# Performance work log

Measured on AMD Instinct MI355X. Metric: run time of the kernel, lower is better.

Reference implementation:

```python
import jax, jax.numpy as jnp
import numpy as np

GRID = 192
ISO = 0.0

CORNERS = [(0,0,0),(1,0,0),(0,1,0),(1,1,0),(0,0,1),(1,0,1),(0,1,1),(1,1,1)]
# 12 cube edges as pairs of corner offsets
EDGES = [
    ((0,0,0),(1,0,0)),((0,1,0),(1,1,0)),((0,0,1),(1,0,1)),((0,1,1),(1,1,1)),
    ((0,0,0),(0,1,0)),((1,0,0),(1,1,0)),((0,0,1),(0,1,1)),((1,0,1),(1,1,1)),
    ((0,0,0),(0,0,1)),((1,0,0),(1,0,1)),((0,1,0),(0,1,1)),((1,1,0),(1,1,1)),
]


def setup_inputs() -> dict:
    key = jax.random.key(0)
    grid = jax.random.normal(key, (GRID, GRID, GRID), dtype=jnp.float32)
    return {"grid": grid}


def _dual_verts(grid, iso):
    # One dual vertex per cell of the padded grid: mean of the iso-crossing
    # points on the cell's 12 edges (dual-marching-cubes vertex placement).
    X, Y, Z = grid.shape
    P = jnp.pad(grid, 1, constant_values=iso + 1.0)  # (X+2, Y+2, Z+2)
    Cx, Cy, Cz = X + 1, Y + 1, Z + 1                 # number of cells per axis
    vals = {c: P[c[0]:c[0]+Cx, c[1]:c[1]+Cy, c[2]:c[2]+Cz] for c in CORNERS}
    sum_pt = jnp.zeros((Cx, Cy, Cz, 3), grid.dtype)
    cnt = jnp.zeros((Cx, Cy, Cz), grid.dtype)
    for ca, cb in EDGES:  # fixed 12-iteration loop, fully vectorized over cells
        vA, vB = vals[ca], vals[cb]
        m = (vA < iso) != (vB < iso)                 # edge crosses isosurface
        t = jnp.where(m, (iso - vA) / jnp.where(m, vB - vA, 1.0), 0.0)
        oa = jnp.asarray(ca, grid.dtype)
        ob = jnp.asarray(cb, grid.dtype)
        pt = oa + t[..., None] * (ob - oa)           # local crossing point
        mf = m.astype(grid.dtype)
        sum_pt = sum_pt + mf[..., None] * pt
        cnt = cnt + mf
    base = jnp.stack(jnp.meshgrid(jnp.arange(Cx), jnp.arange(Cy), jnp.arange(Cz), indexing='ij'), axis=-1).astype(grid.dtype)
    verts = base + sum_pt / jnp.maximum(cnt, 1.0)[..., None]
    # undo +1 padding offset, then normalize by (dim - 1) as in the module
    verts = (verts - 1.0) / (jnp.asarray([X, Y, Z], grid.dtype) - 1.0)
    return verts.reshape(-1, 3), (cnt > 0).reshape(-1)


def _quads(grid, iso):
    # One quad per grid edge that crosses the isosurface, connecting the dual
    # vertices of the 4 cells sharing that edge. Emitted densely with a mask
    # (jit-compatible fixed shapes); masked rows are inactive.
    X, Y, Z = grid.shape
    P = jnp.pad(grid, 1, constant_values=iso + 1.0)
    Cx, Cy, Cz = X + 1, Y + 1, Z + 1
    sgn = P < iso
    def cid(a, b, c):  # flatten cell index
        return (a * Cy + b) * Cz + c
    qs, ms = [], []
    # x-directed edges: shared by cells (i, j-1/j, k-1/k)
    m = sgn[0:Cx, 1:Cy, 1:Cz] != sgn[1:Cx+1, 1:Cy, 1:Cz]
    a = jnp.arange(Cx)[:, None, None]; b = jnp.arange(1, Cy)[None, :, None]; c = jnp.arange(1, Cz)[None, None, :]
    q = jnp.stack(jnp.broadcast_arrays(cid(a, b-1, c-1), cid(a, b, c-1), cid(a, b, c), cid(a, b-1, c)), axis=-1)
    qs.append(q.reshape(-1, 4)); ms.append(m.reshape(-1))
    # y-directed edges: shared by cells (i-1/i, j, k-1/k)
    m = sgn[1:Cx, 0:Cy, 1:Cz] != sgn[1:Cx, 1:Cy+1, 1:Cz]
    a = jnp.arange(1, Cx)[:, None, None]; b = jnp.arange(Cy)[None, :, None]; c = jnp.arange(1, Cz)[None, None, :]
    q = jnp.stack(jnp.broadcast_arrays(cid(a-1, b, c-1), cid(a, b, c-1), cid(a, b, c), cid(a-1, b, c)), axis=-1)
    qs.append(q.reshape(-1, 4)); ms.append(m.reshape(-1))
    # z-directed edges: shared by cells (i-1/i, j-1/j, k)
    m = sgn[1:Cx, 1:Cy, 0:Cz] != sgn[1:Cx, 1:Cy, 1:Cz+1]
    a = jnp.arange(1, Cx)[:, None, None]; b = jnp.arange(1, Cy)[None, :, None]; c = jnp.arange(Cz)[None, None, :]
    q = jnp.stack(jnp.broadcast_arrays(cid(a-1, b-1, c), cid(a, b-1, c), cid(a, b, c), cid(a-1, b, c)), axis=-1)
    qs.append(q.reshape(-1, 4)); ms.append(m.reshape(-1))
    quads = jnp.concatenate(qs, axis=0).astype(jnp.int32)
    qmask = jnp.concatenate(ms, axis=0)
    return quads, qmask


def reference(grid):
    verts, vmask = _dual_verts(grid, ISO)
    quads, qmask = _quads(grid, ISO)
    return verts, vmask, quads, qmask
```

## Files before the change

kernel.cpp:

```cpp
#include <hip/hip_runtime.h>

#define GN 192
#define CN 193
#define CN2 (CN * CN)

#define NV        ((size_t)CN * CN * CN)
#define OFF_VMASK ((size_t)(NV * 3))
#define OFF_QUADS ((size_t)(OFF_VMASK + NV))
#define QSEG      ((size_t)CN * GN * GN)
#define OFF_QMASK ((size_t)(OFF_QUADS + 3 * QSEG * 4))

__device__ __forceinline__ float gpad(const float* __restrict__ g, int x, int y, int z) {
    if ((unsigned)x < (unsigned)GN && (unsigned)y < (unsigned)GN && (unsigned)z < (unsigned)GN)
        return g[((size_t)x * GN + y) * GN + z];
    return 1.0f;
}

__global__ __launch_bounds__(256) void dmc_fused(const float* __restrict__ g,
                                                 float* __restrict__ out) {
    const size_t lin = (size_t)blockIdx.x * 256 + threadIdx.x;
    if (lin >= NV) return;
    const int linI = (int)lin;
    const int k = linI % CN;
    const int t2 = linI / CN;
    const int j = t2 % CN;
    const int i = t2 / CN;

    const float v000 = gpad(g, i - 1, j - 1, k - 1);
    const float v100 = gpad(g, i,     j - 1, k - 1);
    const float v010 = gpad(g, i - 1, j,     k - 1);
    const float v110 = gpad(g, i,     j,     k - 1);
    const float v001 = gpad(g, i - 1, j - 1, k);
    const float v101 = gpad(g, i,     j - 1, k);
    const float v011 = gpad(g, i - 1, j,     k);
    const float v111 = gpad(g, i,     j,     k);

    const bool s000 = v000 < 0.f, s100 = v100 < 0.f, s010 = v010 < 0.f, s110 = v110 < 0.f;
    const bool s001 = v001 < 0.f, s101 = v101 < 0.f, s011 = v011 < 0.f, s111 = v111 < 0.f;

    float sx = 0.f, sy = 0.f, sz = 0.f;
    int cnt = 0;
    auto acc = [&](float vA, float vB, bool sA, bool sB, int axis, float o1, float o2) {
        if (sA != sB) {
            const float t = -vA * __builtin_amdgcn_rcpf(vB - vA);
            if (axis == 0)      { sx += t;  sy += o1; sz += o2; }
            else if (axis == 1) { sx += o1; sy += t;  sz += o2; }
            else                { sx += o1; sy += o2; sz += t;  }
            cnt++;
        }
    };
    acc(v000, v100, s000, s100, 0, 0.f, 0.f);
    acc(v010, v110, s010, s110, 0, 1.f, 0.f);
    acc(v001, v101, s001, s101, 0, 0.f, 1.f);
    acc(v011, v111, s011, s111, 0, 1.f, 1.f);
    acc(v000, v010, s000, s010, 1, 0.f, 0.f);
    acc(v100, v110, s100, s110, 1, 1.f, 0.f);
    acc(v001, v011, s001, s011, 1, 0.f, 1.f);
    acc(v101, v111, s101, s111, 1, 1.f, 1.f);
    acc(v000, v001, s000, s001, 2, 0.f, 0.f);
    acc(v100, v101, s100, s101, 2, 1.f, 0.f);
    acc(v010, v011, s010, s011, 2, 0.f, 1.f);
    acc(v110, v111, s110, s111, 2, 1.f, 1.f);

    const float rc = __builtin_amdgcn_rcpf(fmaxf((float)cnt, 1.0f));
    const float inv191 = 1.0f / 191.0f;
    out[lin * 3 + 0] = ((float)i + sx * rc - 1.0f) * inv191;
    out[lin * 3 + 1] = ((float)j + sy * rc - 1.0f) * inv191;
    out[lin * 3 + 2] = ((float)k + sz * rc - 1.0f) * inv191;
    out[OFF_VMASK + lin] = (cnt > 0) ? 1.0f : 0.0f;

    const float flin = (float)linI;
    float4* const quads = (float4*)(out + OFF_QUADS);
    float* const qmask = out + OFF_QMASK;

    if (j < GN && k < GN) {
        const size_t r = ((size_t)i * GN + j) * GN + k;
        float4 q;
        q.x = flin;
        q.y = flin + (float)CN;
        q.z = flin + (float)(CN+1);
        q.w = flin + 1.0f;
        quads[r] = q;
        qmask[r] = (s011 != s111) ? 1.0f : 0.0f;
    }
    if (i >= 1 && k < GN) {
        const size_t r = QSEG + ((size_t)(i - 1) * CN + j) * GN + k;
        float4 q;
        q.x = flin - (float)CN2;
        q.y = flin;
        q.z = flin + 1.0f;
        q.w = flin - (float)(CN2 - 1);
        quads[r] = q;
        qmask[r] = (s001 != s011) ? 1.0f : 0.0f;
    }
    if (i >= 1 && j >= 1) {
        const size_t r = 2 * QSEG + ((size_t)(i - 1) * GN + (j - 1)) * CN + k;
        float4 q;
        q.x = flin - (float)(CN2 + CN);
        q.y = flin - (float)CN;
        q.z = flin;
        q.w = flin - (float)CN2;
        quads[r] = q;
        qmask[r] = (s000 != s001) ? 1.0f : 0.0f;
    }
}

extern "C" void kernel_launch(void* const* d_in, const int* in_sizes, int n_in,
                              void* d_out, int out_size, void* d_ws, size_t ws_size,
                              hipStream_t stream) {
    const float* g = (const float*)d_in[0];
    float* out = (float*)d_out;
    const int nblocks = (int)((NV + 255) / 256);
    dmc_fused<<<dim3(nblocks), dim3(256), 0, stream>>>(g, out);
}
```

Baseline: 557.3 us.

## Process four z-adjacent cells per thread with vector loads and nontemporal stores

Each thread now handles a run of four cells along z. It loads four 5-element grid rows with vector loads instead of 8 scalar loads per cell, and shares corner values between neighbouring cells. Quad and mask outputs are written with vector nontemporal stores, aiming to cut load instructions and cache pollution in a store-bound kernel. The cost is wider per-lane store strides, which may reduce per-instruction coalescing, plus more register use.

```diff
diff --git a/kernel.cpp b/kernel.cpp
--- a/kernel.cpp
+++ b/kernel.cpp
@@ -3,6 +3,8 @@
 #define GN 192
 #define CN 193
 #define CN2 (CN * CN)
+#define QPOS 49
+#define NPOS ((size_t)CN * CN * QPOS)
 
 #define NV        ((size_t)CN * CN * CN)
 #define OFF_VMASK ((size_t)(NV * 3))
@@ -10,98 +12,132 @@
 #define QSEG      ((size_t)CN * GN * GN)
 #define OFF_QMASK ((size_t)(OFF_QUADS + 3 * QSEG * 4))
 
-__device__ __forceinline__ float gpad(const float* __restrict__ g, int x, int y, int z) {
-    if ((unsigned)x < (unsigned)GN && (unsigned)y < (unsigned)GN && (unsigned)z < (unsigned)GN)
-        return g[((size_t)x * GN + y) * GN + z];
-    return 1.0f;
+typedef float v4f __attribute__((ext_vector_type(4)));
+
+__device__ __forceinline__ void load_row(const float* __restrict__ g, int x, int y,
+                                         int k0, float r[5]) {
+    if ((unsigned)x < (unsigned)GN && (unsigned)y < (unsigned)GN) {
+        const float* rp = g + ((size_t)x * GN + y) * GN;
+        r[0] = (k0 > 0) ? rp[k0 - 1] : 1.0f;
+        if (k0 < GN) {
+            const v4f v = *(const v4f*)(rp + k0);
+            r[1] = v.x; r[2] = v.y; r[3] = v.z; r[4] = v.w;
+        } else {
+            r[1] = r[2] = r[3] = r[4] = 1.0f;
+        }
+    } else {
+        r[0] = r[1] = r[2] = r[3] = r[4] = 1.0f;
+    }
 }
 
 __global__ __launch_bounds__(256) void dmc_fused(const float* __restrict__ g,
                                                  float* __restrict__ out) {
-    const size_t lin = (size_t)blockIdx.x * 256 + threadIdx.x;
-    if (lin >= NV) return;
-    const int linI = (int)lin;
-    const int k = linI % CN;
-    const int t2 = linI / CN;
-    const int j = t2 % CN;
-    const int i = t2 / CN;
+    const size_t t = (size_t)blockIdx.x * 256 + threadIdx.x;
+    if (t >= NPOS) return;
+    const int ti = (int)t;
+    const int q  = ti % QPOS;
+    const int rj = ti / QPOS;
+    const int j  = rj % CN;
+    const int i  = rj / CN;
+    const int k0 = q * 4;
 
-    const float v000 = gpad(g, i - 1, j - 1, k - 1);
-    const float v100 = gpad(g, i,     j - 1, k - 1);
-    const float v010 = gpad(g, i - 1, j,     k - 1);
-    const float v110 = gpad(g, i,     j,     k - 1);
-    const float v001 = gpad(g, i - 1, j - 1, k);
-    const float v101 = gpad(g, i,     j - 1, k);
-    const float v011 = gpad(g, i - 1, j,     k);
-    const float v111 = gpad(g, i,     j,     k);
+    float r00[5], r10[5], r01[5], r11[5];
+    load_row(g, i - 1, j - 1, k0, r00);
+    load_row(g, i,     j - 1, k0, r10);
+    load_row(g, i - 1, j,     k0, r01);
+    load_row(g, i,     j,     k0, r11);
 
-    const bool s000 = v000 < 0.f, s100 = v100 < 0.f, s010 = v010 < 0.f, s110 = v110 < 0.f;
-    const bool s001 = v001 < 0.f, s101 = v101 < 0.f, s011 = v011 < 0.f, s111 = v111 < 0.f;
+    const int ncell = (q < 48) ? 4 : 1;
+    const int cellbase = rj * CN + k0;
+    const float flin0 = (float)cellbase;
 
-    float sx = 0.f, sy = 0.f, sz = 0.f;
-    int cnt = 0;
-    auto acc = [&](float vA, float vB, bool sA, bool sB, int axis, float o1, float o2) {
-        if (sA != sB) {
-            const float t = -vA * __builtin_amdgcn_rcpf(vB - vA);
-            if (axis == 0)      { sx += t;  sy += o1; sz += o2; }
-            else if (axis == 1) { sx += o1; sy += t;  sz += o2; }
-            else                { sx += o1; sy += o2; sz += t;  }
-            cnt++;
+    float mA[4], mB[4], mC[4];
+
+    #pragma unroll
+    for (int c = 0; c < 4; ++c) {
+        const float v000 = r00[c], v001 = r00[c + 1];
+        const float v100 = r10[c], v101 = r10[c + 1];
+        const float v010 = r01[c], v011 = r01[c + 1];
+        const float v110 = r11[c], v111 = r11[c + 1];
+        const bool s000 = v000 < 0.f, s100 = v100 < 0.f, s010 = v010 < 0.f, s110 = v110 < 0.f;
+        const bool s001 = v001 < 0.f, s101 = v101 < 0.f, s011 = v011 < 0.f, s111 = v111 < 0.f;
+
+        mA[c] = (s011 != s111) ? 1.0f : 0.0f;
+        mB[c] = (s001 != s011) ? 1.0f : 0.0f;
+        mC[c] = (s000 != s001) ? 1.0f : 0.0f;
+
+        float sx = 0.f, sy = 0.f, sz = 0.f;
+        int cnt = 0;
+        auto acc = [&](float vA, float vB, bool sA, bool sB, int axis, float o1, float o2) {
+            if (sA != sB) {
+                const float tt = -vA * __builtin_amdgcn_rcpf(vB - vA);
+                if (axis == 0)      { sx += tt; sy += o1; sz += o2; }
+                else if (axis == 1) { sx += o1; sy += tt; sz += o2; }
+                else                { sx += o1; sy += o2; sz += tt; }
+                cnt++;
+            }
+        };
+        acc(v000, v100, s000, s100, 0, 0.f, 0.f);
+        acc(v010, v110, s010, s110, 0, 1.f, 0.f);
+        acc(v001, v101, s001, s101, 0, 0.f, 1.f);
+        acc(v011, v111, s011, s111, 0, 1.f, 1.f);
+        acc(v000, v010, s000, s010, 1, 0.f, 0.f);
+        acc(v100, v110, s100, s110, 1, 1.f, 0.f);
+        acc(v001, v011, s001, s011, 1, 0.f, 1.f);
+        acc(v101, v111, s101, s111, 1, 1.f, 1.f);
+        acc(v000, v001, s000, s001, 2, 0.f, 0.f);
+        acc(v100, v101, s100, s101, 2, 1.f, 0.f);
+        acc(v010, v011, s010, s011, 2, 0.f, 1.f);
+        acc(v110, v111, s110, s111, 2, 1.f, 1.f);
+
+        if (c < ncell) {
+            const float rc = __builtin_amdgcn_rcpf(fmaxf((float)cnt, 1.0f));
+            const float inv191 = 1.0f / 191.0f;
+            const int k = k0 + c;
+            const size_t vb = (size_t)(cellbase + c) * 3;
+            out[vb + 0] = ((float)i + sx * rc - 1.0f) * inv191;
+            out[vb + 1] = ((float)j + sy * rc - 1.0f) * inv191;
+            out[vb + 2] = ((float)k + sz * rc - 1.0f) * inv191;
+            out[OFF_VMASK + cellbase + c] = (cnt > 0) ? 1.0f : 0.0f;
         }
-    };
-    acc(v000, v100, s000, s100, 0, 0.f, 0.f);
-    acc(v010, v110, s010, s110, 0, 1.f, 0.f);
-    acc(v001, v101, s001, s101, 0, 0.f, 1.f);
-    acc(v011, v111, s011, s111, 0, 1.f, 1.f);
-    acc(v000, v010, s000, s010, 1, 0.f, 0.f);
-    acc(v100, v110, s100, s110, 1, 1.f, 0.f);
-    acc(v001, v011, s001, s011, 1, 0.f, 1.f);
-    acc(v101, v111, s101, s111, 1, 1.f, 1.f);
-    acc(v000, v001, s000, s001, 2, 0.f, 0.f);
-    acc(v100, v101, s100, s101, 2, 1.f, 0.f);
-    acc(v010, v011, s010, s011, 2, 0.f, 1.f);
-    acc(v110, v111, s110, s111, 2, 1.f, 1.f);
+    }
 
-    const float rc = __builtin_amdgcn_rcpf(fmaxf((float)cnt, 1.0f));
-    const float inv191 = 1.0f / 191.0f;
-    out[lin * 3 + 0] = ((float)i + sx * rc - 1.0f) * inv191;
-    out[lin * 3 + 1] = ((float)j + sy * rc - 1.0f) * inv191;
-    out[lin * 3 + 2] = ((float)k + sz * rc - 1.0f) * inv191;
-    out[OFF_VMASK + lin] = (cnt > 0) ? 1.0f : 0.0f;
-
-    const float flin = (float)linI;
-    float4* const quads = (float4*)(out + OFF_QUADS);
+    v4f* const quads = (v4f*)(out + OFF_QUADS);
     float* const qmask = out + OFF_QMASK;
 
-    if (j < GN && k < GN) {
-        const size_t r = ((size_t)i * GN + j) * GN + k;
-        float4 q;
-        q.x = flin;
-        q.y = flin + (float)CN;
-        q.z = flin + (float)(CN+1);
-        q.w = flin + 1.0f;
-        quads[r] = q;
-        qmask[r] = (s011 != s111) ? 1.0f : 0.0f;
+    if (j < GN && q < 48) {
+        const size_t rA = ((size_t)i * GN + j) * GN + k0;
+        #pragma unroll
+        for (int c = 0; c < 4; ++c) {
+            const float f = flin0 + (float)c;
+            v4f qd = {f, f + (float)CN, f + (float)(CN + 1), f + 1.0f};
+            __builtin_nontemporal_store(qd, quads + rA + c);
+        }
+        v4f mv = {mA[0], mA[1], mA[2], mA[3]};
+        __builtin_nontemporal_store(mv, (v4f*)(qmask + rA));
     }
-    if (i >= 1 && k < GN) {
-        const size_t r = QSEG + ((size_t)(i - 1) * CN + j) * GN + k;
-        float4 q;
-        q.x = flin - (float)CN2;
-        q.y = flin;
-        q.z = flin + 1.0f;
-        q.w = flin - (float)(CN2 - 1);
-        quads[r] = q;
-        qmask[r] = (s001 != s011) ? 1.0f : 0.0f;
+    if (i >= 1 && q < 48) {
+        const size_t rB = QSEG + ((size_t)(i - 1) * CN + j) * GN + k0;
+        #pragma unroll
+        for (int c = 0; c < 4; ++c) {
+            const float f = flin0 + (float)c;
+            v4f qd = {f - (float)CN2, f, f + 1.0f, f - (float)(CN2 - 1)};
+            __builtin_nontemporal_store(qd, quads + rB + c);
+        }
+        v4f mv = {mB[0], mB[1], mB[2], mB[3]};
+        __builtin_nontemporal_store(mv, (v4f*)(qmask + rB));
     }
     if (i >= 1 && j >= 1) {
-        const size_t r = 2 * QSEG + ((size_t)(i - 1) * GN + (j - 1)) * CN + k;
-        float4 q;
-        q.x = flin - (float)(CN2 + CN);
-        q.y = flin - (float)CN;
-        q.z = flin;
-        q.w = flin - (float)CN2;
-        quads[r] = q;
-        qmask[r] = (s000 != s001) ? 1.0f : 0.0f;
+        const size_t rC = 2 * QSEG + ((size_t)(i - 1) * GN + (j - 1)) * CN + k0;
+        #pragma unroll
+        for (int c = 0; c < 4; ++c) {
+            if (c < ncell) {
+                const float f = flin0 + (float)c;
+                v4f qd = {f - (float)(CN2 + CN), f - (float)CN, f, f - (float)CN2};
+                __builtin_nontemporal_store(qd, quads + rC + c);
+                qmask[rC + c] = mC[c];
+            }
+        }
     }
 }
 
@@ -110,6 +146,6 @@
                               hipStream_t stream) {
     const float* g = (const float*)d_in[0];
     float* out = (float*)d_out;
-    const int nblocks = (int)((NV + 255) / 256);
+    const int nblocks = (int)((NPOS + 255) / 256);
     dmc_fused<<<dim3(nblocks), dim3(256), 0, stream>>>(g, out);
 }
```

New measurement: 1.025 ms. 1.84x slower.
